# Kernel optimization log

Measured on AMD Instinct MI355X. Metric: run time of the kernel, lower is better.

The kernel has to match this reference:

```python
import jax, jax.numpy as jnp
import numpy as np

B, T, C = 2, 2048, 1024
N_HEAD = 16
HEAD_DIM = C // N_HEAD
ROPE_BASE = 10000.0


def setup_inputs() -> dict:
    key = jax.random.key(0)
    ks = jax.random.split(key, 5)
    s = 0.02
    return {
        "x": jax.random.normal(ks[0], (B, T, C), dtype=jnp.float32),
        "Wq": jax.random.normal(ks[1], (C, C), dtype=jnp.float32) * s,
        "Wk": jax.random.normal(ks[2], (C, C), dtype=jnp.float32) * s,
        "Wv": jax.random.normal(ks[3], (C, C), dtype=jnp.float32) * s,
        "Wo": jax.random.normal(ks[4], (C, C), dtype=jnp.float32) * s,
    }


def _rope_cos_sin(seq_len, head_dim, dtype):
    inv_freq = 1.0 / (ROPE_BASE ** (jnp.arange(0, head_dim, 2, dtype=jnp.float32) / head_dim))
    t = jnp.arange(seq_len, dtype=jnp.float32)
    freqs = jnp.einsum("i,j->ij", t, inv_freq)          # [T, head_dim/2]
    emb = jnp.concatenate([freqs, freqs], axis=-1)        # [T, head_dim]
    return jnp.cos(emb).astype(dtype), jnp.sin(emb).astype(dtype)


def _rotate_half(x):
    x1, x2 = jnp.split(x, 2, axis=-1)
    return jnp.concatenate([-x2, x1], axis=-1)


def _mha(x, Wq, Wk, Wv, Wo):
    b, t, c = x.shape
    # torch nn.Linear stores weight [out, in]: y = x @ W.T
    q = (x @ Wq.T).reshape(b, t, N_HEAD, HEAD_DIM).transpose(0, 2, 1, 3)  # [B,H,T,D]
    k = (x @ Wk.T).reshape(b, t, N_HEAD, HEAD_DIM).transpose(0, 2, 1, 3)
    v = (x @ Wv.T).reshape(b, t, N_HEAD, HEAD_DIM).transpose(0, 2, 1, 3)
    cos, sin = _rope_cos_sin(t, HEAD_DIM, x.dtype)        # [T,D] each, broadcast over B,H
    q = q * cos + _rotate_half(q) * sin
    k = k * cos + _rotate_half(k) * sin
    scale = 1.0 / np.sqrt(HEAD_DIM).astype(np.float32)
    att = jnp.einsum("bhqd,bhkd->bhqk", q, k) * scale     # [B,H,T,T]
    causal = jnp.tril(jnp.ones((t, t), dtype=bool))
    att = jnp.where(causal, att, jnp.finfo(att.dtype).min)
    att = jax.nn.softmax(att, axis=-1)
    y = jnp.einsum("bhqk,bhkd->bhqd", att, v)             # [B,H,T,D]
    y = y.transpose(0, 2, 1, 3).reshape(b, t, c)
    return y @ Wo.T


def reference(x, Wq, Wk, Wv, Wo):
    return _mha(x, Wq, Wk, Wv, Wo)
```

## Files before the change

kernel.cpp:

```cpp
#include <hip/hip_runtime.h>

#define BB 2
#define TT 2048
#define CC 1024
#define NH 16
#define HD 64

typedef __attribute__((ext_vector_type(8))) short bf16x8;
typedef __attribute__((ext_vector_type(4))) float floatx4;
typedef __attribute__((ext_vector_type(16))) float floatx16;

__device__ __forceinline__ unsigned short f2bf(float f) {
    union { float f; unsigned int u; } v; v.f = f;
    unsigned int u = v.u;
    u = (u + 0x7fffu + ((u >> 16) & 1u)) >> 16;
    return (unsigned short)u;
}
__device__ __forceinline__ float bf2f(unsigned short u) {
    return __uint_as_float((unsigned)u << 16);
}

typedef __attribute__((address_space(3))) unsigned char* lds_ptr_t;
typedef const __attribute__((address_space(1))) unsigned char* glob_ptr_t;
__device__ __forceinline__ void gll16(const void* g, void* l) {
    __builtin_amdgcn_global_load_lds((glob_ptr_t)g, (lds_ptr_t)l, 16, 0, 0);
}

__global__ __launch_bounds__(256) void cast_all_k(const float* __restrict__ x,
                                                  const float* __restrict__ wq,
                                                  const float* __restrict__ wk,
                                                  const float* __restrict__ wv,
                                                  const float* __restrict__ wo,
                                                  unsigned short* __restrict__ xb,
                                                  unsigned short* __restrict__ wqkvb,
                                                  unsigned short* __restrict__ wob,
                                                  float2* __restrict__ tabQ,
                                                  float2* __restrict__ tabK) {
    if (blockIdx.x >= 8192) {
        int idx = (blockIdx.x - 8192) * 256 + threadIdx.x;
        int t = idx >> 5, j = idx & 31;
        const float C1 = 0.41524101186092f;
        const float I2PI = 0.15915494309189535f;
        float rev = (float)t * (__builtin_amdgcn_exp2f(-(float)j * C1) * I2PI);
        rev -= floorf(rev);
        float ang = rev * 6.2831853071796f;
        float c = __cosf(ang), s = __sinf(ang);
        const float qs = 0.18033688011112f;
        tabK[idx] = make_float2(c, s);
        tabQ[idx] = make_float2(c * qs, s * qs);
        return;
    }
    int i = blockIdx.x * 256 + threadIdx.x;
    const float* src;
    unsigned short* dst;
    if (i < 1048576) {
        src = x + (size_t)i * 4;
        dst = xb + (size_t)i * 4;
    } else {
        int w   = (i - 1048576) >> 18;
        int off = (i - 1048576) & 262143;
        const float* s0 = (w == 0) ? wq : (w == 1) ? wk : (w == 2) ? wv : wo;
        unsigned short* d0 = (w == 3) ? wob : (wqkvb + (size_t)w * 1048576);
        src = s0 + (size_t)off * 4;
        dst = d0 + (size_t)off * 4;
    }
    float4 v = *(const float4*)src;
    ushort4 o;
    o.x = f2bf(v.x); o.y = f2bf(v.y); o.z = f2bf(v.z); o.w = f2bf(v.w);
    *(ushort4*)dst = o;
}

__global__ __launch_bounds__(256) void gemm128_k(const unsigned short* __restrict__ A,
                                                 const unsigned short* __restrict__ Bt,
                                                 float* __restrict__ C, int N, int K) {
    __shared__ __align__(16) unsigned short As[128][64];
    __shared__ __align__(16) unsigned short Bs[128][64];
    const int tid  = threadIdx.x;
    const int wave = tid >> 6;
    const int lane = tid & 63;
    const int quad = lane >> 4;
    const int l16  = lane & 15;
    const int sw   = l16 & 7;
    const int wr = (wave >> 1) * 64;
    const int wc = (wave & 1) * 64;
    const int bid = blockIdx.x;
    const int xcd = bid & 7, sl = bid >> 3;
    const int row0 = (xcd * 4 + (sl >> 3)) * 128;
    const int col0 = (sl & 7) * 128;
    const int w8r = wave * 8 + (lane >> 3);
    const int cg  = ((lane & 7) ^ (lane >> 3)) * 8;
    const int cl  = (lane & 7) * 8;

    const unsigned short* Ap = A  + (size_t)(row0 + w8r) * K + cg;
    const unsigned short* Bp = Bt + (size_t)(col0 + w8r) * K + cg;

    floatx4 acc[4][4];
    #pragma unroll
    for (int i = 0; i < 4; i++)
        #pragma unroll
        for (int j = 0; j < 4; j++) acc[i][j] = (floatx4){0.f, 0.f, 0.f, 0.f};

    for (int k0 = 0; k0 < K; k0 += 64) {
        __syncthreads();
        #pragma unroll
        for (int isu = 0; isu < 4; isu++) {
            gll16(Ap + (size_t)(isu * 32) * K + k0, &As[isu * 32 + w8r][cl]);
            gll16(Bp + (size_t)(isu * 32) * K + k0, &Bs[isu * 32 + w8r][cl]);
        }
        __syncthreads();
        #pragma unroll
        for (int kk = 0; kk < 2; kk++) {
            bf16x8 af[4], bfr[4];
            #pragma unroll
            for (int i = 0; i < 4; i++)
                af[i]  = *(const bf16x8*)&As[wr + 16 * i + l16][((kk * 4 + quad) ^ sw) * 8];
            #pragma unroll
            for (int j = 0; j < 4; j++)
                bfr[j] = *(const bf16x8*)&Bs[wc + 16 * j + l16][((kk * 4 + quad) ^ sw) * 8];
            #pragma unroll
            for (int i = 0; i < 4; i++)
                #pragma unroll
                for (int j = 0; j < 4; j++)
                    acc[i][j] = __builtin_amdgcn_mfma_f32_16x16x32_bf16(af[i], bfr[j], acc[i][j], 0, 0, 0);
        }
    }

    #pragma unroll
    for (int i = 0; i < 4; i++)
        #pragma unroll
        for (int j = 0; j < 4; j++)
            #pragma unroll
            for (int r = 0; r < 4; r++) {
                int row = row0 + wr + 16 * i + quad * 4 + r;
                int col = col0 + wc + 16 * j + l16;
                C[(size_t)row * N + col] = acc[i][j][r];
            }
}

__global__ __launch_bounds__(256) void gemm_qkv_k(const unsigned short* __restrict__ A,
                                                  const unsigned short* __restrict__ Bt,
                                                  const float2* __restrict__ tabQ,
                                                  const float2* __restrict__ tabK,
                                                  unsigned short* __restrict__ Qb,
                                                  unsigned short* __restrict__ Kb,
                                                  unsigned short* __restrict__ Vb) {
    __shared__ __align__(16) unsigned short SMEM[128 * 128];
    unsigned short (*As)[64] = (unsigned short(*)[64])SMEM;
    unsigned short (*Bs)[64] = (unsigned short(*)[64])(SMEM + 128 * 64);
    unsigned short (*Eb)[128] = (unsigned short(*)[128])SMEM;
    const int K = 1024;
    const int tid  = threadIdx.x;
    const int wave = tid >> 6;
    const int lane = tid & 63;
    const int quad = lane >> 4;
    const int l16  = lane & 15;
    const int sw   = l16 & 7;
    const int wr = (wave >> 1) * 64;
    const int wc = (wave & 1) * 64;
    const int bid = blockIdx.x;
    const int xcd = bid & 7, sl = bid >> 3;
    const int row0 = (xcd * 4 + sl / 24) * 128;
    const int col0 = (sl % 24) * 128;
    const int w8r = wave * 8 + (lane >> 3);
    const int cg  = ((lane & 7) ^ (lane >> 3)) * 8;
    const int cl  = (lane & 7) * 8;

    const unsigned short* Ap = A  + (size_t)(row0 + w8r) * K + cg;
    const unsigned short* Bp = Bt + (size_t)(col0 + w8r) * K + cg;

    floatx4 acc[4][4];
    #pragma unroll
    for (int i = 0; i < 4; i++)
        #pragma unroll
        for (int j = 0; j < 4; j++) acc[i][j] = (floatx4){0.f, 0.f, 0.f, 0.f};

    for (int k0 = 0; k0 < K; k0 += 64) {
        __syncthreads();
        #pragma unroll
        for (int isu = 0; isu < 4; isu++) {
            gll16(Ap + (size_t)(isu * 32) * K + k0, &As[isu * 32 + w8r][cl]);
            gll16(Bp + (size_t)(isu * 32) * K + k0, &Bs[isu * 32 + w8r][cl]);
        }
        __syncthreads();
        #pragma unroll
        for (int kk = 0; kk < 2; kk++) {
            bf16x8 af[4], bfr[4];
            #pragma unroll
            for (int i = 0; i < 4; i++)
                af[i]  = *(const bf16x8*)&As[wr + 16 * i + l16][((kk * 4 + quad) ^ sw) * 8];
            #pragma unroll
            for (int j = 0; j < 4; j++)
                bfr[j] = *(const bf16x8*)&Bs[wc + 16 * j + l16][((kk * 4 + quad) ^ sw) * 8];
            #pragma unroll
            for (int i = 0; i < 4; i++)
                #pragma unroll
                for (int j = 0; j < 4; j++)
                    acc[i][j] = __builtin_amdgcn_mfma_f32_16x16x32_bf16(af[i], bfr[j], acc[i][j], 0, 0, 0);
        }
    }

    __syncthreads();
    #pragma unroll
    for (int i = 0; i < 4; i++)
        #pragma unroll
        for (int j = 0; j < 4; j++)
            #pragma unroll
            for (int r = 0; r < 4; r++) {
                int erow = wr + 16 * i + quad * 4 + r;
                int col  = wc + 16 * j + l16;
                int pcol = (((col >> 3) ^ (erow & 15)) << 3) | (col & 7);
                Eb[erow][pcol] = f2bf(acc[i][j][r]);
            }
    __syncthreads();

    const int row  = tid >> 1;
    const int half = tid & 1;
    const int grow = row0 + row;
    const int t    = grow & (TT - 1);
    const int bb   = grow >> 11;
    const int sect = col0 >> 10;
    const int hh   = ((col0 & 1023) >> 6) + half;
    union { int4 q[8]; unsigned short u[64]; } raw;
    #pragma unroll
    for (int i = 0; i < 8; i++) {
        int pg = (half * 8 + i) ^ (row & 15);
        raw.q[i] = *(const int4*)&Eb[row][pg << 3];
    }
    size_t obase = ((size_t)(bb * NH + hh) * TT + t) * 64;
    if (sect == 2) {
        #pragma unroll
        for (int i = 0; i < 8; i++) *(int4*)(Vb + obase + 8 * i) = raw.q[i];
    } else {
        const float4* tab = (const float4*)((sect ? tabK : tabQ) + (size_t)t * 32);
        unsigned short* dst = sect ? Kb : Qb;
        union { int4 q[8]; unsigned short u[64]; } o;
        #pragma unroll
        for (int i = 0; i < 16; i++) {
            float4 cs = tab[i];
            int j0 = 2 * i, j1 = 2 * i + 1;
            float a0 = bf2f(raw.u[j0]), b0 = bf2f(raw.u[j0 + 32]);
            float a1 = bf2f(raw.u[j1]), b1 = bf2f(raw.u[j1 + 32]);
            o.u[j0]      = f2bf(a0 * cs.x - b0 * cs.y);
            o.u[j0 + 32] = f2bf(b0 * cs.x + a0 * cs.y);
            o.u[j1]      = f2bf(a1 * cs.z - b1 * cs.w);
            o.u[j1 + 32] = f2bf(b1 * cs.z + a1 * cs.w);
        }
        #pragma unroll
        for (int i = 0; i < 8; i++) *(int4*)(dst + obase + 8 * i) = o.q[i];
    }
}

__global__ __launch_bounds__(256) void vtr_k(const unsigned short* __restrict__ Vb,
                                             unsigned short* __restrict__ Vt) {
    __shared__ __align__(16) unsigned short Vsh[64][70];
    const int tid = threadIdx.x;
    const int tt = blockIdx.x;
    const int bh = blockIdx.y;
    const int sr = tid >> 2;
    const int sc = (tid & 3) * 16;
    const unsigned short* src = Vb + ((size_t)bh * TT + tt * 64 + sr) * 64 + sc;
    *(int4*)&Vsh[sr][sc]     = *(const int4*)src;
    *(int4*)&Vsh[sr][sc + 8] = *(const int4*)(src + 8);
    __syncthreads();
    const int dr = tid >> 2;
    const int tc = (tid & 3) * 16;
    unsigned short tv[16];
    #pragma unroll
    for (int i = 0; i < 16; i++) {
        int x = tc + i;
        int key = (x & ~15) + (x & 3) + ((x >> 2) & 1) * 8 + ((x >> 3) & 1) * 4;
        tv[i] = Vsh[key][dr];
    }
    size_t vo = ((size_t)bh * 64 + dr) * TT + tt * 64 + tc;
    *(int4*)(Vt + vo)     = *(int4*)&tv[0];
    *(int4*)(Vt + vo + 8) = *(int4*)&tv[8];
}

__global__ __launch_bounds__(256, 4) void flash_k(const unsigned short* __restrict__ Qb,
                                                  const unsigned short* __restrict__ Kb,
                                                  const unsigned short* __restrict__ Vt,
                                                  unsigned short* __restrict__ O0,
                                                  unsigned short* __restrict__ O1,
                                                  float* __restrict__ L0, float* __restrict__ L1) {
    __shared__ __align__(16) unsigned short Ks[64][72];
    __shared__ __align__(16) unsigned short Vs[64][72];
    const int tid  = threadIdx.x;
    const int wave = tid >> 6;
    const int lane = tid & 63;
    const int h    = lane >> 5;
    const int l32  = lane & 31;
    const int qt    = 15 - (blockIdx.x >> 6);
    const int inner = blockIdx.x & 63;
    const int bh    = inner >> 1;
    const int split = inner & 1;
    const int q0 = qt * 128;
    const int qw = q0 + wave * 32 + l32;
    const int sr = tid >> 2;
    const int sc = (tid & 3) * 16;

    bf16x8 qf[4];
    {
        const unsigned short* qp = Qb + ((size_t)bh * TT + qw) * 64 + h * 8;
        #pragma unroll
        for (int kk = 0; kk < 4; kk++) qf[kk] = *(const bf16x8*)(qp + kk * 16);
    }

    floatx16 accO[2];
    accO[0] = (floatx16)(0.f);
    accO[1] = (floatx16)(0.f);
    float lsum = 0.f;

    const int kt0 = split * (qt + 1);
    const int kt1 = kt0 + qt + 1;
    const unsigned short* kbase = Kb + (size_t)bh * TT * 64;
    const unsigned short* vbase = Vt + (size_t)bh * 64 * TT;

    const unsigned short* kp = kbase + ((size_t)(kt0 * 64) + sr) * 64 + sc;
    const unsigned short* vp = vbase + (size_t)sr * TT + kt0 * 64 + sc;
    int4 ka = *(const int4*)kp, kb2 = *(const int4*)(kp + 8);
    int4 va = *(const int4*)vp, vb2 = *(const int4*)(vp + 8);

    for (int kt = kt0; kt < kt1; kt++) {
        __syncthreads();
        *(int4*)&Ks[sr][sc]     = ka;
        *(int4*)&Ks[sr][sc + 8] = kb2;
        *(int4*)&Vs[sr][sc]     = va;
        *(int4*)&Vs[sr][sc + 8] = vb2;
        __syncthreads();
        if (kt + 1 < kt1) {
            const unsigned short* kp2 = kbase + ((size_t)((kt + 1) * 64) + sr) * 64 + sc;
            const unsigned short* vp2 = vbase + (size_t)sr * TT + (kt + 1) * 64 + sc;
            ka  = *(const int4*)kp2; kb2 = *(const int4*)(kp2 + 8);
            va  = *(const int4*)vp2; vb2 = *(const int4*)(vp2 + 8);
        }

        const bool diag = (kt >= 2 * qt);
        bf16x8 pfrag[4];

        #pragma unroll
        for (int mb = 0; mb < 2; mb++) {
            floatx16 sacc = (floatx16)(0.f);
            #pragma unroll
            for (int kk = 0; kk < 4; kk++) {
                bf16x8 kf = *(const bf16x8*)&Ks[32 * mb + l32][kk * 16 + h * 8];
                sacc = __builtin_amdgcn_mfma_f32_32x32x16_bf16(kf, qf[kk], sacc, 0, 0, 0);
            }
            float p[16];
            const int kmb = kt * 64 + 32 * mb + 4 * h;
            #pragma unroll
            for (int r = 0; r < 16; r++) {
                float pv = __builtin_amdgcn_exp2f(sacc[r]);
                if (diag) {
                    int ki = kmb + (r & 3) + 8 * (r >> 2);
                    if (ki > qw) pv = 0.f;
                }
                lsum += pv;
                p[r] = pv;
            }
            #pragma unroll
            for (int half = 0; half < 2; half++) {
                union { bf16x8 v; unsigned u[4]; } pk;
                #pragma unroll
                for (int i = 0; i < 4; i++) {
                    unsigned ulo = __float_as_uint(p[half * 8 + 2 * i]);
                    unsigned uhi = __float_as_uint(p[half * 8 + 2 * i + 1]);
                    pk.u[i] = (ulo >> 16) | (uhi & 0xffff0000u);
                }
                pfrag[2 * mb + half] = pk.v;
            }
        }

        #pragma unroll
        for (int mbo = 0; mbo < 2; mbo++) {
            #pragma unroll
            for (int kk = 0; kk < 4; kk++) {
                bf16x8 vf = *(const bf16x8*)&Vs[32 * mbo + l32][kk * 16 + h * 8];
                accO[mbo] = __builtin_amdgcn_mfma_f32_32x32x16_bf16(vf, pfrag[kk], accO[mbo], 0, 0, 0);
            }
        }
    }

    lsum += __shfl_xor(lsum, 32);
    unsigned short* Op = split ? O1 : O0;
    float* Lp = split ? L1 : L0;
    if (lane < 32) Lp[(size_t)bh * TT + qw] = lsum;
    unsigned short* orow = Op + ((size_t)bh * TT + qw) * 64;
    #pragma unroll
    for (int mbo = 0; mbo < 2; mbo++)
        #pragma unroll
        for (int a = 0; a < 4; a++) {
            ushort4 o4;
            o4.x = f2bf(accO[mbo][4 * a + 0]);
            o4.y = f2bf(accO[mbo][4 * a + 1]);
            o4.z = f2bf(accO[mbo][4 * a + 2]);
            o4.w = f2bf(accO[mbo][4 * a + 3]);
            *(ushort4*)(orow + 32 * mbo + 8 * a + 4 * h) = o4;
        }
}

__global__ __launch_bounds__(256) void combine_k(const unsigned short* __restrict__ O0,
                                                 const unsigned short* __restrict__ O1,
                                                 const float* __restrict__ L0,
                                                 const float* __restrict__ L1,
                                                 unsigned short* __restrict__ Yb) {
    int idx = blockIdx.x * 256 + threadIdx.x;
    int dg  = idx & 15;
    int row = idx >> 4;
    float inv = 1.0f / (L0[row] + L1[row]);
    uint2 a = ((const uint2*)O0)[idx];
    uint2 b = ((const uint2*)O1)[idx];
    float a0 = __uint_as_float(a.x << 16),      b0 = __uint_as_float(b.x << 16);
    float a1 = __uint_as_float(a.x & 0xffff0000u), b1 = __uint_as_float(b.x & 0xffff0000u);
    float a2 = __uint_as_float(a.y << 16),      b2 = __uint_as_float(b.y << 16);
    float a3 = __uint_as_float(a.y & 0xffff0000u), b3 = __uint_as_float(b.y & 0xffff0000u);
    ushort4 o;
    o.x = f2bf((a0 + b0) * inv);
    o.y = f2bf((a1 + b1) * inv);
    o.z = f2bf((a2 + b2) * inv);
    o.w = f2bf((a3 + b3) * inv);
    int bh = row >> 11, t = row & (TT - 1);
    int bb = bh >> 4, hh = bh & 15;
    *(ushort4*)(Yb + ((size_t)(bb * TT + t)) * CC + hh * 64 + dg * 4) = o;
}

extern "C" void kernel_launch(void* const* d_in, const int* in_sizes, int n_in,
                              void* d_out, int out_size, void* d_ws, size_t ws_size,
                              hipStream_t stream) {
    (void)in_sizes; (void)n_in; (void)out_size; (void)ws_size;
    const float* x  = (const float*)d_in[0];
    const float* Wq = (const float*)d_in[1];
    const float* Wk = (const float*)d_in[2];
    const float* Wv = (const float*)d_in[3];
    const float* Wo = (const float*)d_in[4];
    float* out = (float*)d_out;
    char* ws = (char*)d_ws;

    unsigned short* xb    = (unsigned short*)(ws + 0);
    unsigned short* wqkvb = (unsigned short*)(ws + (8ull  << 20));
    unsigned short* wob   = (unsigned short*)(ws + (14ull << 20));
    unsigned short* Qb    = (unsigned short*)(ws + (16ull << 20));
    unsigned short* Kb    = (unsigned short*)(ws + (24ull << 20));
    unsigned short* Vb    = (unsigned short*)(ws + (32ull << 20));
    unsigned short* Vt    = (unsigned short*)(ws + (40ull << 20));
    unsigned short* Yb    = (unsigned short*)(ws + (48ull << 20));
    unsigned short* O0    = (unsigned short*)(ws + (56ull << 20));
    unsigned short* O1    = (unsigned short*)(ws + (64ull << 20));
    float* L0 = (float*)(ws + (72ull << 20));
    float* L1 = (float*)(ws + (72ull << 20) + (256ull << 10));
    float2* tabQ = (float2*)(ws + (73ull << 20));
    float2* tabK = (float2*)(ws + (73ull << 20) + (512ull << 10));

    cast_all_k<<<8448, 256, 0, stream>>>(x, Wq, Wk, Wv, Wo, xb, wqkvb, wob, tabQ, tabK);
    gemm_qkv_k<<<768, 256, 0, stream>>>(xb, wqkvb, tabQ, tabK, Qb, Kb, Vb);
    vtr_k<<<dim3(32, 32), 256, 0, stream>>>(Vb, Vt);
    flash_k<<<1024, 256, 0, stream>>>(Qb, Kb, Vt, O0, O1, L0, L1);
    combine_k<<<4096, 256, 0, stream>>>(O0, O1, L0, L1, Yb);
    gemm128_k<<<256, 256, 0, stream>>>(Yb, wob, out, 1024, 1024);
}
```

Baseline: 180.4 us.

## Fuse V transpose into QKV GEMM epilogue and double flash query tile

The QKV GEMM epilogue now writes V directly in transposed, key-permuted layout, removing the separate vtr_k kernel and its round trip of V through global memory. The flash kernel now handles 256 query rows per block, with each wave processing two 32-row query slices that share each loaded K/V fragment. This halves the grid and lowers launch bounds to 2 blocks per CU. It raises register pressure and lowers occupancy in exchange for more reuse of K/V per LDS load. The epilogue's V path also does 64 scalar LDS reads per thread.

```diff
diff --git a/kernel.cpp b/kernel.cpp
--- a/kernel.cpp
+++ b/kernel.cpp
@@ -143,7 +143,7 @@
                                                   const float2* __restrict__ tabK,
                                                   unsigned short* __restrict__ Qb,
                                                   unsigned short* __restrict__ Kb,
-                                                  unsigned short* __restrict__ Vb) {
+                                                  unsigned short* __restrict__ Vt) {
     __shared__ __align__(16) unsigned short SMEM[128 * 128];
     unsigned short (*As)[64] = (unsigned short(*)[64])SMEM;
     unsigned short (*Bs)[64] = (unsigned short(*)[64])(SMEM + 128 * 64);
@@ -213,24 +213,38 @@
             }
     __syncthreads();
 
-    const int row  = tid >> 1;
-    const int half = tid & 1;
-    const int grow = row0 + row;
-    const int t    = grow & (TT - 1);
-    const int bb   = grow >> 11;
     const int sect = col0 >> 10;
-    const int hh   = ((col0 & 1023) >> 6) + half;
-    union { int4 q[8]; unsigned short u[64]; } raw;
-    #pragma unroll
-    for (int i = 0; i < 8; i++) {
-        int pg = (half * 8 + i) ^ (row & 15);
-        raw.q[i] = *(const int4*)&Eb[row][pg << 3];
-    }
-    size_t obase = ((size_t)(bb * NH + hh) * TT + t) * 64;
+    const int bbB  = row0 >> 11;
     if (sect == 2) {
-        #pragma unroll
-        for (int i = 0; i < 8; i++) *(int4*)(Vb + obase + 8 * i) = raw.q[i];
+        const int colv  = tid >> 1;
+        const int tpart = tid & 1;
+        const int d     = colv & 63;
+        const int head  = ((col0 - 2048) >> 6) + (colv >> 6);
+        const int bh    = bbB * NH + head;
+        const int t0g   = (row0 & (TT - 1)) + tpart * 64;
+        unsigned short tv[64];
+        #pragma unroll
+        for (int i = 0; i < 64; i++) {
+            int lk  = tpart * 64 + (i & ~15) + (i & 3) + ((i >> 2) & 1) * 8 + ((i >> 3) & 1) * 4;
+            int pg  = (colv >> 3) ^ (lk & 15);
+            tv[i] = Eb[lk][(pg << 3) | (colv & 7)];
+        }
+        unsigned short* vdst = Vt + ((size_t)bh * 64 + d) * TT + t0g;
+        #pragma unroll
+        for (int i = 0; i < 8; i++) *(int4*)(vdst + 8 * i) = *(int4*)&tv[8 * i];
     } else {
+        const int row  = tid >> 1;
+        const int half = tid & 1;
+        const int grow = row0 + row;
+        const int t    = grow & (TT - 1);
+        const int hh   = ((col0 & 1023) >> 6) + half;
+        union { int4 q[8]; unsigned short u[64]; } raw;
+        #pragma unroll
+        for (int i = 0; i < 8; i++) {
+            int pg = (half * 8 + i) ^ (row & 15);
+            raw.q[i] = *(const int4*)&Eb[row][pg << 3];
+        }
+        size_t obase = ((size_t)(bbB * NH + hh) * TT + t) * 64;
         const float4* tab = (const float4*)((sect ? tabK : tabQ) + (size_t)t * 32);
         unsigned short* dst = sect ? Kb : Qb;
         union { int4 q[8]; unsigned short u[64]; } o;
@@ -250,33 +264,7 @@
     }
 }
 
-__global__ __launch_bounds__(256) void vtr_k(const unsigned short* __restrict__ Vb,
-                                             unsigned short* __restrict__ Vt) {
-    __shared__ __align__(16) unsigned short Vsh[64][70];
-    const int tid = threadIdx.x;
-    const int tt = blockIdx.x;
-    const int bh = blockIdx.y;
-    const int sr = tid >> 2;
-    const int sc = (tid & 3) * 16;
-    const unsigned short* src = Vb + ((size_t)bh * TT + tt * 64 + sr) * 64 + sc;
-    *(int4*)&Vsh[sr][sc]     = *(const int4*)src;
-    *(int4*)&Vsh[sr][sc + 8] = *(const int4*)(src + 8);
-    __syncthreads();
-    const int dr = tid >> 2;
-    const int tc = (tid & 3) * 16;
-    unsigned short tv[16];
-    #pragma unroll
-    for (int i = 0; i < 16; i++) {
-        int x = tc + i;
-        int key = (x & ~15) + (x & 3) + ((x >> 2) & 1) * 8 + ((x >> 3) & 1) * 4;
-        tv[i] = Vsh[key][dr];
-    }
-    size_t vo = ((size_t)bh * 64 + dr) * TT + tt * 64 + tc;
-    *(int4*)(Vt + vo)     = *(int4*)&tv[0];
-    *(int4*)(Vt + vo + 8) = *(int4*)&tv[8];
-}
-
-__global__ __launch_bounds__(256, 4) void flash_k(const unsigned short* __restrict__ Qb,
+__global__ __launch_bounds__(256, 2) void flash_k(const unsigned short* __restrict__ Qb,
                                                   const unsigned short* __restrict__ Kb,
                                                   const unsigned short* __restrict__ Vt,
                                                   unsigned short* __restrict__ O0,
@@ -289,29 +277,32 @@
     const int lane = tid & 63;
     const int h    = lane >> 5;
     const int l32  = lane & 31;
-    const int qt    = 15 - (blockIdx.x >> 6);
+    const int qt    = 7 - (blockIdx.x >> 6);
     const int inner = blockIdx.x & 63;
     const int bh    = inner >> 1;
     const int split = inner & 1;
-    const int q0 = qt * 128;
-    const int qw = q0 + wave * 32 + l32;
+    const int q0 = qt * 256;
+    const int qwb = q0 + wave * 64;
     const int sr = tid >> 2;
     const int sc = (tid & 3) * 16;
 
-    bf16x8 qf[4];
-    {
-        const unsigned short* qp = Qb + ((size_t)bh * TT + qw) * 64 + h * 8;
-        #pragma unroll
-        for (int kk = 0; kk < 4; kk++) qf[kk] = *(const bf16x8*)(qp + kk * 16);
-    }
-
-    floatx16 accO[2];
-    accO[0] = (floatx16)(0.f);
-    accO[1] = (floatx16)(0.f);
-    float lsum = 0.f;
-
-    const int kt0 = split * (qt + 1);
-    const int kt1 = kt0 + qt + 1;
+    bf16x8 qf[2][4];
+    #pragma unroll
+    for (int qs = 0; qs < 2; qs++) {
+        const unsigned short* qp = Qb + ((size_t)bh * TT + qwb + qs * 32 + l32) * 64 + h * 8;
+        #pragma unroll
+        for (int kk = 0; kk < 4; kk++) qf[qs][kk] = *(const bf16x8*)(qp + kk * 16);
+    }
+
+    floatx16 accO[2][2];
+    #pragma unroll
+    for (int qs = 0; qs < 2; qs++)
+        #pragma unroll
+        for (int mbo = 0; mbo < 2; mbo++) accO[qs][mbo] = (floatx16)(0.f);
+    float lsum[2] = {0.f, 0.f};
+
+    const int kt0 = split * (2 * qt + 2);
+    const int kt1 = kt0 + 2 * qt + 2;
     const unsigned short* kbase = Kb + (size_t)bh * TT * 64;
     const unsigned short* vbase = Vt + (size_t)bh * 64 * TT;
 
@@ -334,68 +325,82 @@
             va  = *(const int4*)vp2; vb2 = *(const int4*)(vp2 + 8);
         }
 
-        const bool diag = (kt >= 2 * qt);
-        bf16x8 pfrag[4];
+        const bool diag = (kt >= 4 * qt);
+        bf16x8 pfrag[2][4];
 
         #pragma unroll
         for (int mb = 0; mb < 2; mb++) {
-            floatx16 sacc = (floatx16)(0.f);
-            #pragma unroll
-            for (int kk = 0; kk < 4; kk++) {
-                bf16x8 kf = *(const bf16x8*)&Ks[32 * mb + l32][kk * 16 + h * 8];
-                sacc = __builtin_amdgcn_mfma_f32_32x32x16_bf16(kf, qf[kk], sacc, 0, 0, 0);
+            bf16x8 kf[4];
+            #pragma unroll
+            for (int kk = 0; kk < 4; kk++)
+                kf[kk] = *(const bf16x8*)&Ks[32 * mb + l32][kk * 16 + h * 8];
+            #pragma unroll
+            for (int qs = 0; qs < 2; qs++) {
+                floatx16 sacc = (floatx16)(0.f);
+                #pragma unroll
+                for (int kk = 0; kk < 4; kk++)
+                    sacc = __builtin_amdgcn_mfma_f32_32x32x16_bf16(kf[kk], qf[qs][kk], sacc, 0, 0, 0);
+                float p[16];
+                const int kmb = kt * 64 + 32 * mb + 4 * h;
+                const int qw  = qwb + qs * 32 + l32;
+                #pragma unroll
+                for (int r = 0; r < 16; r++) {
+                    float pv = __builtin_amdgcn_exp2f(sacc[r]);
+                    if (diag) {
+                        int ki = kmb + (r & 3) + 8 * (r >> 2);
+                        if (ki > qw) pv = 0.f;
+                    }
+                    lsum[qs] += pv;
+                    p[r] = pv;
+                }
+                #pragma unroll
+                for (int hf = 0; hf < 2; hf++) {
+                    union { bf16x8 v; unsigned u[4]; } pk;
+                    #pragma unroll
+                    for (int i = 0; i < 4; i++) {
+                        unsigned ulo = __float_as_uint(p[hf * 8 + 2 * i]);
+                        unsigned uhi = __float_as_uint(p[hf * 8 + 2 * i + 1]);
+                        pk.u[i] = (ulo >> 16) | (uhi & 0xffff0000u);
+                    }
+                    pfrag[qs][2 * mb + hf] = pk.v;
+                }
             }
-            float p[16];
-            const int kmb = kt * 64 + 32 * mb + 4 * h;
-            #pragma unroll
-            for (int r = 0; r < 16; r++) {
-                float pv = __builtin_amdgcn_exp2f(sacc[r]);
-                if (diag) {
-                    int ki = kmb + (r & 3) + 8 * (r >> 2);
-                    if (ki > qw) pv = 0.f;
-                }
-                lsum += pv;
-                p[r] = pv;
-            }
-            #pragma unroll
-            for (int half = 0; half < 2; half++) {
-                union { bf16x8 v; unsigned u[4]; } pk;
-                #pragma unroll
-                for (int i = 0; i < 4; i++) {
-                    unsigned ulo = __float_as_uint(p[half * 8 + 2 * i]);
-                    unsigned uhi = __float_as_uint(p[half * 8 + 2 * i + 1]);
-                    pk.u[i] = (ulo >> 16) | (uhi & 0xffff0000u);
-                }
-                pfrag[2 * mb + half] = pk.v;
-            }
         }
 
         #pragma unroll
         for (int mbo = 0; mbo < 2; mbo++) {
-            #pragma unroll
-            for (int kk = 0; kk < 4; kk++) {
-                bf16x8 vf = *(const bf16x8*)&Vs[32 * mbo + l32][kk * 16 + h * 8];
-                accO[mbo] = __builtin_amdgcn_mfma_f32_32x32x16_bf16(vf, pfrag[kk], accO[mbo], 0, 0, 0);
-            }
-        }
-    }
-
-    lsum += __shfl_xor(lsum, 32);
+            bf16x8 vf[4];
+            #pragma unroll
+            for (int kk = 0; kk < 4; kk++)
+                vf[kk] = *(const bf16x8*)&Vs[32 * mbo + l32][kk * 16 + h * 8];
+            #pragma unroll
+            for (int qs = 0; qs < 2; qs++)
+                #pragma unroll
+                for (int kk = 0; kk < 4; kk++)
+                    accO[qs][mbo] = __builtin_amdgcn_mfma_f32_32x32x16_bf16(vf[kk], pfrag[qs][kk], accO[qs][mbo], 0, 0, 0);
+        }
+    }
+
     unsigned short* Op = split ? O1 : O0;
     float* Lp = split ? L1 : L0;
-    if (lane < 32) Lp[(size_t)bh * TT + qw] = lsum;
-    unsigned short* orow = Op + ((size_t)bh * TT + qw) * 64;
-    #pragma unroll
-    for (int mbo = 0; mbo < 2; mbo++)
-        #pragma unroll
-        for (int a = 0; a < 4; a++) {
-            ushort4 o4;
-            o4.x = f2bf(accO[mbo][4 * a + 0]);
-            o4.y = f2bf(accO[mbo][4 * a + 1]);
-            o4.z = f2bf(accO[mbo][4 * a + 2]);
-            o4.w = f2bf(accO[mbo][4 * a + 3]);
-            *(ushort4*)(orow + 32 * mbo + 8 * a + 4 * h) = o4;
-        }
+    #pragma unroll
+    for (int qs = 0; qs < 2; qs++) {
+        float l = lsum[qs] + __shfl_xor(lsum[qs], 32);
+        const int qw = qwb + qs * 32 + l32;
+        if (lane < 32) Lp[(size_t)bh * TT + qw] = l;
+        unsigned short* orow = Op + ((size_t)bh * TT + qw) * 64;
+        #pragma unroll
+        for (int mbo = 0; mbo < 2; mbo++)
+            #pragma unroll
+            for (int a = 0; a < 4; a++) {
+                ushort4 o4;
+                o4.x = f2bf(accO[qs][mbo][4 * a + 0]);
+                o4.y = f2bf(accO[qs][mbo][4 * a + 1]);
+                o4.z = f2bf(accO[qs][mbo][4 * a + 2]);
+                o4.w = f2bf(accO[qs][mbo][4 * a + 3]);
+                *(ushort4*)(orow + 32 * mbo + 8 * a + 4 * h) = o4;
+            }
+    }
 }
 
 __global__ __launch_bounds__(256) void combine_k(const unsigned short* __restrict__ O0,
@@ -440,20 +445,18 @@
     unsigned short* wob   = (unsigned short*)(ws + (14ull << 20));
     unsigned short* Qb    = (unsigned short*)(ws + (16ull << 20));
     unsigned short* Kb    = (unsigned short*)(ws + (24ull << 20));
-    unsigned short* Vb    = (unsigned short*)(ws + (32ull << 20));
-    unsigned short* Vt    = (unsigned short*)(ws + (40ull << 20));
-    unsigned short* Yb    = (unsigned short*)(ws + (48ull << 20));
-    unsigned short* O0    = (unsigned short*)(ws + (56ull << 20));
-    unsigned short* O1    = (unsigned short*)(ws + (64ull << 20));
-    float* L0 = (float*)(ws + (72ull << 20));
-    float* L1 = (float*)(ws + (72ull << 20) + (256ull << 10));
-    float2* tabQ = (float2*)(ws + (73ull << 20));
-    float2* tabK = (float2*)(ws + (73ull << 20) + (512ull << 10));
+    unsigned short* Vt    = (unsigned short*)(ws + (32ull << 20));
+    unsigned short* Yb    = (unsigned short*)(ws + (40ull << 20));
+    unsigned short* O0    = (unsigned short*)(ws + (48ull << 20));
+    unsigned short* O1    = (unsigned short*)(ws + (56ull << 20));
+    float* L0 = (float*)(ws + (64ull << 20));
+    float* L1 = (float*)(ws + (64ull << 20) + (256ull << 10));
+    float2* tabQ = (float2*)(ws + (65ull << 20));
+    float2* tabK = (float2*)(ws + (65ull << 20) + (512ull << 10));
 
     cast_all_k<<<8448, 256, 0, stream>>>(x, Wq, Wk, Wv, Wo, xb, wqkvb, wob, tabQ, tabK);
-    gemm_qkv_k<<<768, 256, 0, stream>>>(xb, wqkvb, tabQ, tabK, Qb, Kb, Vb);
-    vtr_k<<<dim3(32, 32), 256, 0, stream>>>(Vb, Vt);
-    flash_k<<<1024, 256, 0, stream>>>(Qb, Kb, Vt, O0, O1, L0, L1);
+    gemm_qkv_k<<<768, 256, 0, stream>>>(xb, wqkvb, tabQ, tabK, Qb, Kb, Vt);
+    flash_k<<<512, 256, 0, stream>>>(Qb, Kb, Vt, O0, O1, L0, L1);
     combine_k<<<4096, 256, 0, stream>>>(O0, O1, L0, L1, Yb);
     gemm128_k<<<256, 256, 0, stream>>>(Yb, wob, out, 1024, 1024);
 }
```

Result: slower. 197.5 us (+9.5%).
